# Kernel tuning notes

Measured on AMD Instinct MI355X. Metric: run time of the kernel, lower is better.

The kernel has to match this reference:

```python
import math
import jax, jax.numpy as jnp
import numpy as np

N_EMBD = 1024
N_HEAD = 16
HEAD_DIM = N_EMBD // N_HEAD
B, T = 4, 2048
LN_EPS = 1e-5


def setup_inputs() -> dict:
    key = jax.random.key(0)
    ks = jax.random.split(key, 20)
    s = 0.02
    d = {
        'x': jax.random.normal(ks[0], (B, T, N_EMBD), jnp.float32),
        'Wq': jax.random.normal(ks[1], (N_EMBD, N_EMBD), jnp.float32) * s,
        'bq': jnp.zeros((N_EMBD,), jnp.float32),
        'Wk': jax.random.normal(ks[2], (N_EMBD, N_EMBD), jnp.float32) * s,
        'bk': jnp.zeros((N_EMBD,), jnp.float32),
        'Wv': jax.random.normal(ks[3], (N_EMBD, N_EMBD), jnp.float32) * s,
        'bv': jnp.zeros((N_EMBD,), jnp.float32),
        'Wo': jax.random.normal(ks[4], (N_EMBD, N_EMBD), jnp.float32) * s,
        'bo': jnp.zeros((N_EMBD,), jnp.float32),
        'ln1_g': jnp.ones((N_EMBD,), jnp.float32),
        'ln1_b': jnp.zeros((N_EMBD,), jnp.float32),
        'ln2_g': jnp.ones((N_EMBD,), jnp.float32),
        'ln2_b': jnp.zeros((N_EMBD,), jnp.float32),
        'W_fc': jax.random.normal(ks[5], (N_EMBD, 4 * N_EMBD), jnp.float32) * s,
        'b_fc': jnp.zeros((4 * N_EMBD,), jnp.float32),
        'W_proj': jax.random.normal(ks[6], (4 * N_EMBD, N_EMBD), jnp.float32) * s,
        'b_proj': jnp.zeros((N_EMBD,), jnp.float32),
    }
    return d


def _layernorm(x, g, b):
    mu = jnp.mean(x, axis=-1, keepdims=True)
    var = jnp.var(x, axis=-1, keepdims=True)
    return (x - mu) * jax.lax.rsqrt(var + LN_EPS) * g + b


def _new_gelu(x):
    c = math.sqrt(2.0 / math.pi)
    return 0.5 * x * (1.0 + jnp.tanh(c * (x + 0.044715 * x ** 3)))


def _attn(x, Wq, bq, Wk, bk, Wv, bv, Wo, bo):
    Bq, Tq, C = x.shape
    def heads(y):  # (B,T,C) -> (B,H,T,D)
        return y.reshape(Bq, Tq, N_HEAD, HEAD_DIM).transpose(0, 2, 1, 3)
    q = heads(x @ Wq + bq)
    k = heads(x @ Wk + bk)
    v = heads(x @ Wv + bv)
    scores = jnp.einsum('bhqd,bhkd->bhqk', q, k) / math.sqrt(HEAD_DIM)
    causal = jnp.tril(jnp.ones((Tq, Tq), bool))
    scores = jnp.where(causal, scores, -jnp.inf)
    w = jax.nn.softmax(scores, axis=-1)
    av = jnp.einsum('bhqk,bhkd->bhqd', w, v)
    av = av.transpose(0, 2, 1, 3).reshape(Bq, Tq, C)
    return av @ Wo + bo


def reference(x, Wq, bq, Wk, bk, Wv, bv, Wo, bo, ln1_g, ln1_b, ln2_g, ln2_b, W_fc, b_fc, W_proj, b_proj):
    x = x + _attn(_layernorm(x, ln1_g, ln1_b), Wq, bq, Wk, bk, Wv, bv, Wo, bo)
    h = _layernorm(x, ln2_g, ln2_b)
    x = x + (_new_gelu(h @ W_fc + b_fc) @ W_proj + b_proj)
    return x
```

## Files before the change

kernel.cpp:

```cpp
#include <hip/hip_runtime.h>

typedef __attribute__((ext_vector_type(8))) short short8;
typedef __attribute__((ext_vector_type(4))) short short4v;
typedef __attribute__((ext_vector_type(4))) float floatx4;
typedef unsigned short u16;

#define MFMA16(a,b,c) __builtin_amdgcn_mfma_f32_16x16x32_bf16(a,b,c,0,0,0)

typedef const __attribute__((address_space(1))) void* gas1;
typedef __attribute__((address_space(3))) void* las3;
static __device__ __forceinline__ void glds16(const void* g, void* l){
  __builtin_amdgcn_global_load_lds((gas1)g, (las3)l, 16, 0, 0);
}

static __device__ __forceinline__ u16 f2b(float f){
  union { float f; unsigned int u; } c; c.f = f;
  unsigned int u = c.u;
  u += 0x7fffu + ((u >> 16) & 1u);
  return (u16)(u >> 16);
}

__global__ __launch_bounds__(256) void transpose_cvt(
    const float* __restrict__ W, u16* __restrict__ Wt, int K, int N){
  __shared__ float tile[32][33];
  const int tx = threadIdx.x & 31;
  const int ty = threadIdx.x >> 5;
  const int nx = blockIdx.x * 32, kx = blockIdx.y * 32;
  #pragma unroll
  for (int i = ty; i < 32; i += 8)
    tile[i][tx] = W[(size_t)(kx + i) * N + nx + tx];
  __syncthreads();
  #pragma unroll
  for (int i = ty; i < 32; i += 8)
    Wt[(size_t)(nx + i) * K + kx + tx] = f2b(tile[tx][i]);
}

__global__ __launch_bounds__(256) void ln_kernel(
    const float* __restrict__ x, const float* __restrict__ g,
    const float* __restrict__ b, u16* __restrict__ out){
  const int row = blockIdx.x, tid = threadIdx.x;
  const float4 v = reinterpret_cast<const float4*>(x + (size_t)row * 1024)[tid];
  float s  = v.x + v.y + v.z + v.w;
  float s2 = v.x*v.x + v.y*v.y + v.z*v.z + v.w*v.w;
  #pragma unroll
  for (int off = 1; off < 64; off <<= 1){
    s  += __shfl_xor(s,  off);
    s2 += __shfl_xor(s2, off);
  }
  __shared__ float red[8];
  const int wave = tid >> 6, lane = tid & 63;
  if (lane == 0){ red[wave] = s; red[4 + wave] = s2; }
  __syncthreads();
  s  = red[0] + red[1] + red[2] + red[3];
  s2 = red[4] + red[5] + red[6] + red[7];
  const float mu  = s * (1.f/1024.f);
  const float var = s2 * (1.f/1024.f) - mu * mu;
  const float rs  = rsqrtf(var + 1e-5f);
  const float4 gg = reinterpret_cast<const float4*>(g)[tid];
  const float4 bb = reinterpret_cast<const float4*>(b)[tid];
  ushort4 o;
  o.x = f2b((v.x - mu) * rs * gg.x + bb.x);
  o.y = f2b((v.y - mu) * rs * gg.y + bb.y);
  o.z = f2b((v.z - mu) * rs * gg.z + bb.z);
  o.w = f2b((v.w - mu) * rs * gg.w + bb.w);
  reinterpret_cast<ushort4*>(out + (size_t)row * 1024)[tid] = o;
}

__global__ __launch_bounds__(256) void bias_concat(
    const float* __restrict__ bq, const float* __restrict__ bk,
    const float* __restrict__ bv, float* __restrict__ o){
  const int i = blockIdx.x * 256 + threadIdx.x;
  if (i < 1024) o[i] = bq[i];
  else if (i < 2048) o[i] = bk[i - 1024];
  else if (i < 3072) o[i] = bv[i - 2048];
}

template<bool GELU, bool RES, bool OUTBF, bool QKVMODE>
__global__ __launch_bounds__(256) void gemm128(
    const u16* __restrict__ A, const u16* __restrict__ Bt,
    const float* __restrict__ bias,
    const float* __restrict__ res,
    float* __restrict__ outF, u16* __restrict__ outB,
    u16* __restrict__ vtb,
    int M, int N, int K)
{
  __shared__ __attribute__((aligned(16))) u16 sA[2][128 * 32];
  __shared__ __attribute__((aligned(16))) u16 sB[2][128 * 32];
  const int tid  = threadIdx.x;
  const int wave = tid >> 6, lane = tid & 63, quad = lane >> 4, l16 = lane & 15;
  const int m0 = blockIdx.x * 128, n0 = blockIdx.y * 128;
  const int wm = (wave >> 1) * 64, wn = (wave & 1) * 64;

  const int scol = ((lane & 3) ^ ((lane >> 3) & 3)) * 8;
  const size_t aoff  = (size_t)(m0 + wave*32 + (lane >> 2)) * K + scol;
  const size_t aoff2 = aoff + (size_t)16 * K;
  const int brow = n0 + (wave >> 1)*64 + 4*(lane >> 2) + (wave & 1)*2;
  const size_t boff  = (size_t)brow * K + scol;
  const size_t boff2 = boff + (size_t)K;
  u16* alp = sA[0] + wave * 1024;
  u16* blp = sB[0] + wave * 1024;
  const int qx = (quad ^ ((l16 >> 1) & 3)) * 8;

  floatx4 acc[4][4];
  #pragma unroll
  for (int i = 0; i < 4; i++)
    #pragma unroll
    for (int nt = 0; nt < 4; nt++) acc[i][nt] = floatx4{0.f,0.f,0.f,0.f};

  glds16(A  + aoff,  alp);
  glds16(A  + aoff2, alp + 512);
  glds16(Bt + boff,  blp);
  glds16(Bt + boff2, blp + 512);

  int buf = 0;
  for (int k0 = 0; k0 < K; k0 += 32, buf ^= 1){
    __syncthreads();
    if (k0 + 32 < K){
      const int kn = k0 + 32;
      const int bo = (buf ^ 1) * 4096;
      glds16(A  + aoff  + kn, alp + bo);
      glds16(A  + aoff2 + kn, alp + bo + 512);
      glds16(Bt + boff  + kn, blp + bo);
      glds16(Bt + boff2 + kn, blp + bo + 512);
    }
    const u16* sa = sA[buf];
    const u16* sb = sB[buf];
    short8 af[4], bf[4];
    #pragma unroll
    for (int i = 0; i < 4; i++)
      af[i] = *reinterpret_cast<const short8*>(&sa[(wm + i*16 + l16)*32 + qx]);
    #pragma unroll
    for (int nt = 0; nt < 4; nt++)
      bf[nt] = *reinterpret_cast<const short8*>(&sb[(wn + nt*16 + l16)*32 + qx]);
    #pragma unroll
    for (int i = 0; i < 4; i++)
      #pragma unroll
      for (int nt = 0; nt < 4; nt++)
        acc[i][nt] = MFMA16(af[i], bf[nt], acc[i][nt]);
  }

  const int col0 = n0 + wn + 4*l16;
  const floatx4 bi = *reinterpret_cast<const floatx4*>(&bias[col0]);

  if (QKVMODE && n0 >= 2048){
    #pragma unroll
    for (int nt = 0; nt < 4; nt++){
      const int hd = col0 + nt - 2048;
      u16* vcol = vtb + (size_t)(hd >> 6) * 131072 + (size_t)(hd & 63) * 2048;
      #pragma unroll
      for (int i = 0; i < 4; i++){
        const int t0 = m0 + wm + i*16 + quad*4;
        const int bb = t0 >> 11, tt = t0 & 2047;
        short4v pk;
        #pragma unroll
        for (int r = 0; r < 4; r++) pk[r] = (short)f2b(acc[i][nt][r] + bi[nt]);
        *reinterpret_cast<short4v*>(vcol + (size_t)bb * 2097152 + tt) = pk;
      }
    }
    return;
  }

  #pragma unroll
  for (int i = 0; i < 4; i++){
    #pragma unroll
    for (int r = 0; r < 4; r++){
      const int row = m0 + wm + i*16 + quad*4 + r;
      if (OUTBF){
        short4v o;
        #pragma unroll
        for (int nt = 0; nt < 4; nt++){
          float val = acc[i][nt][r] + bi[nt];
          if (GELU){
            const float t = 0.7978845608028654f * (val + 0.044715f * val * val * val);
            val = val / (1.f + __expf(-2.f * t));
          }
          o[nt] = (short)f2b(val);
        }
        *reinterpret_cast<short4v*>(&outB[(size_t)row * N + col0]) = o;
      } else {
        floatx4 v;
        #pragma unroll
        for (int nt = 0; nt < 4; nt++) v[nt] = acc[i][nt][r] + bi[nt];
        if (RES){
          const floatx4 rr = *reinterpret_cast<const floatx4*>(&res[(size_t)row * N + col0]);
          #pragma unroll
          for (int nt = 0; nt < 4; nt++) v[nt] += rr[nt];
        }
        *reinterpret_cast<floatx4*>(&outF[(size_t)row * N + col0]) = v;
      }
    }
  }
}

__global__ __launch_bounds__(256) void attn_kernel(
    const u16* __restrict__ qkv, const u16* __restrict__ vtb,
    u16* __restrict__ O)
{
  constexpr int T = 2048, LDQ = 3072, LDP = 72;
  __shared__ __attribute__((aligned(16))) u16 sK[2][2][64*32];
  __shared__ __attribute__((aligned(16))) u16 sV[2][2][64*32];
  __shared__ __attribute__((aligned(16))) u16 sP[4][16*LDP];

  const int tid = threadIdx.x, wave = tid >> 6, lane = tid & 63;
  const int quad = lane >> 4, l16 = lane & 15;

  const int lin = blockIdx.y * 16 + blockIdx.x;
  const int j = lin & 15;
  const int bh = lin >> 4;
  const int kk4 = bh >> 4;
  const int jj = (j + ((kk4 & 2) << 2)) & 15;
  const int qt = (kk4 & 1) ? (15 - jj) : jj;
  const int q0 = qt * 128;
  const int b = bh >> 4, h = bh & 15;

  const u16* Qp = qkv + (size_t)b * T * LDQ + h * 64;
  const u16* Kp = Qp + 1024;
  const u16* Vt = vtb + (size_t)bh * 64 * T;

  const int qx = (quad ^ ((l16 >> 1) & 3)) * 8;

  int qg[2]; qg[0] = q0 + wave*16 + l16; qg[1] = qg[0] + 64;
  short8 qf[2][2];
  #pragma unroll
  for (int g = 0; g < 2; g++){
    qf[g][0] = *reinterpret_cast<const short8*>(&Qp[(size_t)qg[g]*LDQ + quad*8]);
    qf[g][1] = *reinterpret_cast<const short8*>(&Qp[(size_t)qg[g]*LDQ + 32 + quad*8]);
  }

  float m_i[2] = {-INFINITY, -INFINITY}, l_i[2] = {0.f, 0.f};
  floatx4 o_acc[2][4];
  #pragma unroll
  for (int g = 0; g < 2; g++)
    #pragma unroll
    for (int nt = 0; nt < 4; nt++) o_acc[g][nt] = floatx4{0.f,0.f,0.f,0.f};

  const int srow = wave*16 + (lane >> 2);
  const int scol = ((lane & 3) ^ ((lane >> 3) & 3)) * 8;
  const int asrc = (lane & 48) | (quad * 4);

  const int kend = q0 + 128;

  {
    glds16(Kp + (size_t)srow*LDQ + scol,      sK[0][0] + wave*512);
    glds16(Kp + (size_t)srow*LDQ + 32 + scol, sK[0][1] + wave*512);
    glds16(Vt + (size_t)srow*T + scol,        sV[0][0] + wave*512);
    glds16(Vt + (size_t)srow*T + 32 + scol,   sV[0][1] + wave*512);
  }

  int buf = 0;
  for (int k0 = 0; k0 < kend; k0 += 64, buf ^= 1){
    __syncthreads();
    if (k0 + 64 < kend){
      const int kn = k0 + 64;
      glds16(Kp + (size_t)(kn + srow)*LDQ + scol,      sK[buf^1][0] + wave*512);
      glds16(Kp + (size_t)(kn + srow)*LDQ + 32 + scol, sK[buf^1][1] + wave*512);
      glds16(Vt + (size_t)srow*T + kn + scol,          sV[buf^1][0] + wave*512);
      glds16(Vt + (size_t)srow*T + kn + 32 + scol,     sV[buf^1][1] + wave*512);
    }

    #pragma unroll
    for (int g = 0; g < 2; g++){
      if (g == 0 && k0 > q0) continue;

      float s[4][4];
      #pragma unroll
      for (int sub = 0; sub < 4; sub++){
        floatx4 sa = floatx4{0.f,0.f,0.f,0.f};
        const short8 kf0 = *reinterpret_cast<const short8*>(&sK[buf][0][(sub*16 + l16)*32 + qx]);
        const short8 kf1 = *reinterpret_cast<const short8*>(&sK[buf][1][(sub*16 + l16)*32 + qx]);
        sa = MFMA16(kf0, qf[g][0], sa);
        sa = MFMA16(kf1, qf[g][1], sa);
        #pragma unroll
        for (int r = 0; r < 4; r++) s[sub][r] = sa[r];
      }
      if (k0 == q0 + g*64){
        #pragma unroll
        for (int sub = 0; sub < 4; sub++)
          #pragma unroll
          for (int r = 0; r < 4; r++){
            const int kidx = k0 + sub*16 + quad*4 + r;
            if (kidx > qg[g]) s[sub][r] = -1e30f;
          }
      }

      float mx = s[0][0];
      #pragma unroll
      for (int sub = 0; sub < 4; sub++)
        #pragma unroll
        for (int r = 0; r < 4; r++) mx = fmaxf(mx, s[sub][r]);
      mx = fmaxf(mx, __shfl_xor(mx, 16));
      mx = fmaxf(mx, __shfl_xor(mx, 32));
      const float mnew  = fmaxf(m_i[g], mx);
      const float alpha = __expf(0.125f * (m_i[g] - mnew));
      float p[4][4], rowsum = 0.f;
      #pragma unroll
      for (int sub = 0; sub < 4; sub++)
        #pragma unroll
        for (int r = 0; r < 4; r++){
          p[sub][r] = __expf(0.125f * (s[sub][r] - mnew));
          rowsum += p[sub][r];
        }
      rowsum += __shfl_xor(rowsum, 16);
      rowsum += __shfl_xor(rowsum, 32);
      l_i[g] = l_i[g] * alpha + rowsum;
      m_i[g] = mnew;

      float arow[4];
      #pragma unroll
      for (int r = 0; r < 4; r++) arow[r] = __shfl(alpha, asrc + r);
      #pragma unroll
      for (int nt = 0; nt < 4; nt++)
        #pragma unroll
        for (int r = 0; r < 4; r++) o_acc[g][nt][r] *= arow[r];

      #pragma unroll
      for (int sub = 0; sub < 4; sub++){
        short4v pk;
        pk[0] = (short)f2b(p[sub][0]); pk[1] = (short)f2b(p[sub][1]);
        pk[2] = (short)f2b(p[sub][2]); pk[3] = (short)f2b(p[sub][3]);
        *reinterpret_cast<short4v*>(&sP[wave][l16*LDP + sub*16 + quad*4]) = pk;
      }
      const short8 pf0 = *reinterpret_cast<const short8*>(&sP[wave][l16*LDP + quad*8]);
      const short8 pf1 = *reinterpret_cast<const short8*>(&sP[wave][l16*LDP + 32 + quad*8]);
      #pragma unroll
      for (int nt = 0; nt < 4; nt++){
        const short8 vf0 = *reinterpret_cast<const short8*>(&sV[buf][0][(nt*16 + l16)*32 + qx]);
        const short8 vf1 = *reinterpret_cast<const short8*>(&sV[buf][1][(nt*16 + l16)*32 + qx]);
        o_acc[g][nt] = MFMA16(pf0, vf0, o_acc[g][nt]);
        o_acc[g][nt] = MFMA16(pf1, vf1, o_acc[g][nt]);
      }
    }
  }

  #pragma unroll
  for (int g = 0; g < 2; g++){
    float lrow[4];
    #pragma unroll
    for (int r = 0; r < 4; r++) lrow[r] = __shfl(l_i[g], asrc + r);
    #pragma unroll
    for (int nt = 0; nt < 4; nt++){
      #pragma unroll
      for (int r = 0; r < 4; r++){
        const int row = q0 + g*64 + wave*16 + quad*4 + r;
        O[(size_t)(b*T + row)*1024 + h*64 + nt*16 + l16] = f2b(o_acc[g][nt][r] / lrow[r]);
      }
    }
  }
}

extern "C" void kernel_launch(void* const* d_in, const int* in_sizes, int n_in,
                              void* d_out, int out_size, void* d_ws, size_t ws_size,
                              hipStream_t stream){
  const float* x      = (const float*)d_in[0];
  const float* Wq     = (const float*)d_in[1];
  const float* bq     = (const float*)d_in[2];
  const float* Wk     = (const float*)d_in[3];
  const float* bk     = (const float*)d_in[4];
  const float* Wv     = (const float*)d_in[5];
  const float* bv     = (const float*)d_in[6];
  const float* Wo     = (const float*)d_in[7];
  const float* bo     = (const float*)d_in[8];
  const float* ln1_g  = (const float*)d_in[9];
  const float* ln1_b  = (const float*)d_in[10];
  const float* ln2_g  = (const float*)d_in[11];
  const float* ln2_b  = (const float*)d_in[12];
  const float* W_fc   = (const float*)d_in[13];
  const float* b_fc   = (const float*)d_in[14];
  const float* W_proj = (const float*)d_in[15];
  const float* b_proj = (const float*)d_in[16];
  float* out = (float*)d_out;
  char* ws = (char*)d_ws;
  const size_t MB = 1024 * 1024;

  u16* bufA  = (u16*)(ws);
  u16* qkvb  = (u16*)(ws + 16*MB);
  u16* vtb   = (u16*)(ws + 64*MB);
  u16* fcb   = (u16*)(ws + 16*MB);
  float* x2  = out;
  u16* Wqkvt = (u16*)(ws + 80*MB);
  u16* Wot   = (u16*)(ws + 86*MB);
  u16* Wfct  = (u16*)(ws + 88*MB);
  u16* Wpjt  = (u16*)(ws + 96*MB);
  float* bqkv= (float*)(ws + 104*MB);

  dim3 tb(256);
  transpose_cvt<<<dim3(32, 32),  tb, 0, stream>>>(Wq,     Wqkvt,             1024, 1024);
  transpose_cvt<<<dim3(32, 32),  tb, 0, stream>>>(Wk,     Wqkvt + 1024*1024, 1024, 1024);
  transpose_cvt<<<dim3(32, 32),  tb, 0, stream>>>(Wv,     Wqkvt + 2048*1024, 1024, 1024);
  transpose_cvt<<<dim3(32, 32),  tb, 0, stream>>>(Wo,     Wot,               1024, 1024);
  transpose_cvt<<<dim3(128, 32), tb, 0, stream>>>(W_fc,   Wfct,              1024, 4096);
  transpose_cvt<<<dim3(32, 128), tb, 0, stream>>>(W_proj, Wpjt,              4096, 1024);
  bias_concat<<<dim3(12), tb, 0, stream>>>(bq, bk, bv, bqkv);

  ln_kernel<<<8192, tb, 0, stream>>>(x, ln1_g, ln1_b, bufA);

  gemm128<false,false,true,true><<<dim3(64,24), tb, 0, stream>>>(
      bufA, Wqkvt, bqkv, nullptr, nullptr, qkvb, vtb, 8192, 3072, 1024);

  attn_kernel<<<dim3(16, 64), tb, 0, stream>>>(qkvb, vtb, bufA);

  gemm128<false,true,false,false><<<dim3(64,8), tb, 0, stream>>>(
      bufA, Wot, bo, x, x2, nullptr, nullptr, 8192, 1024, 1024);

  ln_kernel<<<8192, tb, 0, stream>>>(x2, ln2_g, ln2_b, bufA);

  gemm128<true,false,true,false><<<dim3(64,32), tb, 0, stream>>>(
      bufA, Wfct, b_fc, nullptr, nullptr, fcb, nullptr, 8192, 4096, 1024);

  gemm128<false,true,false,false><<<dim3(64,8), tb, 0, stream>>>(
      fcb, Wpjt, b_proj, x2, out, nullptr, nullptr, 8192, 1024, 4096);
}
```

Measured before the change: 547.2 us.

## Replace 128x128 GEMM with 256x256 tiled 8-wave kernel using fine-grained barrier scheduling

The GEMM kernel moves from a 128x128 tile with 4 waves to a 256x256 tile with 8 waves. Each stage loads a K=64 slice into double-buffered LDS, and the compute is split into interleaved LDS-read and MFMA phases separated by barriers and s_setprio. This raises arithmetic intensity per LDS byte and aims to overlap loads with MFMA. The cost is far fewer blocks (128 for the N=1024 GEMMs), which can leave CUs idle, plus higher register pressure from the 8x4 accumulators.

```diff
diff --git a/kernel.cpp b/kernel.cpp
--- a/kernel.cpp
+++ b/kernel.cpp
@@ -76,7 +76,7 @@
 }
 
 template<bool GELU, bool RES, bool OUTBF, bool QKVMODE>
-__global__ __launch_bounds__(256) void gemm128(
+__global__ __launch_bounds__(512) void gemm256(
     const u16* __restrict__ A, const u16* __restrict__ Bt,
     const float* __restrict__ bias,
     const float* __restrict__ res,
@@ -84,62 +84,93 @@
     u16* __restrict__ vtb,
     int M, int N, int K)
 {
-  __shared__ __attribute__((aligned(16))) u16 sA[2][128 * 32];
-  __shared__ __attribute__((aligned(16))) u16 sB[2][128 * 32];
+  __shared__ __attribute__((aligned(16))) u16 sA[2][2][256 * 32];
+  __shared__ __attribute__((aligned(16))) u16 sB[2][2][256 * 32];
   const int tid  = threadIdx.x;
-  const int wave = tid >> 6, lane = tid & 63, quad = lane >> 4, l16 = lane & 15;
-  const int m0 = blockIdx.x * 128, n0 = blockIdx.y * 128;
-  const int wm = (wave >> 1) * 64, wn = (wave & 1) * 64;
+  const int wave = tid >> 6, lane = tid & 63, ql = lane >> 4, l16 = lane & 15;
+  const int wr = wave >> 2, wc = wave & 3;
+  const int m0 = blockIdx.x * 256, n0 = blockIdx.y * 256;
 
   const int scol = ((lane & 3) ^ ((lane >> 3) & 3)) * 8;
-  const size_t aoff  = (size_t)(m0 + wave*32 + (lane >> 2)) * K + scol;
-  const size_t aoff2 = aoff + (size_t)16 * K;
-  const int brow = n0 + (wave >> 1)*64 + 4*(lane >> 2) + (wave & 1)*2;
-  const size_t boff  = (size_t)brow * K + scol;
-  const size_t boff2 = boff + (size_t)K;
-  u16* alp = sA[0] + wave * 1024;
-  u16* blp = sB[0] + wave * 1024;
-  const int qx = (quad ^ ((l16 >> 1) & 3)) * 8;
-
-  floatx4 acc[4][4];
-  #pragma unroll
-  for (int i = 0; i < 4; i++)
+  const u16* aBase = A  + (size_t)(m0 + wave*16 + (lane >> 2)) * K + scol;
+  const u16* bBase = Bt + (size_t)(n0 + wr*64 + 4*(lane >> 2) + wc) * K + scol;
+  const size_t hK = (size_t)128 * K;
+  const int qx = (ql ^ ((l16 >> 1) & 3)) * 8;
+
+  floatx4 acc[8][4];
+  #pragma unroll
+  for (int i = 0; i < 8; i++)
     #pragma unroll
     for (int nt = 0; nt < 4; nt++) acc[i][nt] = floatx4{0.f,0.f,0.f,0.f};
-
-  glds16(A  + aoff,  alp);
-  glds16(A  + aoff2, alp + 512);
-  glds16(Bt + boff,  blp);
-  glds16(Bt + boff2, blp + 512);
-
-  int buf = 0;
-  for (int k0 = 0; k0 < K; k0 += 32, buf ^= 1){
-    __syncthreads();
-    if (k0 + 32 < K){
-      const int kn = k0 + 32;
-      const int bo = (buf ^ 1) * 4096;
-      glds16(A  + aoff  + kn, alp + bo);
-      glds16(A  + aoff2 + kn, alp + bo + 512);
-      glds16(Bt + boff  + kn, blp + bo);
-      glds16(Bt + boff2 + kn, blp + bo + 512);
-    }
-    const u16* sa = sA[buf];
-    const u16* sb = sB[buf];
-    short8 af[4], bf[4];
-    #pragma unroll
-    for (int i = 0; i < 4; i++)
-      af[i] = *reinterpret_cast<const short8*>(&sa[(wm + i*16 + l16)*32 + qx]);
-    #pragma unroll
-    for (int nt = 0; nt < 4; nt++)
-      bf[nt] = *reinterpret_cast<const short8*>(&sb[(wn + nt*16 + l16)*32 + qx]);
-    #pragma unroll
-    for (int i = 0; i < 4; i++)
-      #pragma unroll
-      for (int nt = 0; nt < 4; nt++)
-        acc[i][nt] = MFMA16(af[i], bf[nt], acc[i][nt]);
-  }
-
-  const int col0 = n0 + wn + 4*l16;
+  short8 af[4], bf[4];
+
+#define STAGE(B_, T_) do { \
+    const size_t ko_ = (size_t)(T_) * 64; \
+    glds16(aBase + ko_,           &sA[B_][0][wave*512]); \
+    glds16(aBase + ko_ + 32,      &sA[B_][1][wave*512]); \
+    glds16(aBase + ko_ + hK,      &sA[B_][0][4096 + wave*512]); \
+    glds16(aBase + ko_ + hK + 32, &sA[B_][1][4096 + wave*512]); \
+    glds16(bBase + ko_,           &sB[B_][0][wave*512]); \
+    glds16(bBase + ko_ + 32,      &sB[B_][1][wave*512]); \
+    glds16(bBase + ko_ + hK,      &sB[B_][0][4096 + wave*512]); \
+    glds16(bBase + ko_ + hK + 32, &sB[B_][1][4096 + wave*512]); \
+  } while(0)
+#define LDA(B_, KH_, Q_) do { \
+    _Pragma("unroll") \
+    for (int ii_ = 0; ii_ < 4; ii_++) \
+      af[ii_] = *reinterpret_cast<const short8*>( \
+          &sA[B_][KH_][(wr*128 + (Q_)*64 + ii_*16 + l16)*32 + qx]); \
+  } while(0)
+#define LDB(B_, KH_) do { \
+    _Pragma("unroll") \
+    for (int nt_ = 0; nt_ < 4; nt_++) \
+      bf[nt_] = *reinterpret_cast<const short8*>( \
+          &sB[B_][KH_][(wc*64 + nt_*16 + l16)*32 + qx]); \
+  } while(0)
+#define MM(Q_) do { \
+    __builtin_amdgcn_s_setprio(1); \
+    _Pragma("unroll") \
+    for (int ii_ = 0; ii_ < 4; ii_++) \
+      _Pragma("unroll") \
+      for (int nt_ = 0; nt_ < 4; nt_++) \
+        acc[(Q_)*4 + ii_][nt_] = MFMA16(af[ii_], bf[nt_], acc[(Q_)*4 + ii_][nt_]); \
+    __builtin_amdgcn_s_setprio(0); \
+  } while(0)
+#define BAR() do { asm volatile("" ::: "memory"); \
+    __builtin_amdgcn_s_barrier(); asm volatile("" ::: "memory"); } while(0)
+#define WAITV(N_) asm volatile("s_waitcnt vmcnt(" #N_ ")" ::: "memory")
+
+  const int ntile = K >> 6;
+  STAGE(0, 0);
+
+  #pragma unroll 1
+  for (int t = 0; t < ntile; t += 2){
+    STAGE(1, t + 1);
+    WAITV(8);
+    BAR();
+    LDB(0, 0); LDA(0, 0, 0); MM(0);
+    BAR();
+    LDA(0, 0, 1); BAR(); MM(1); BAR();
+    LDB(0, 1); LDA(0, 1, 0); BAR(); MM(0); BAR();
+    LDA(0, 1, 1); BAR(); MM(1); BAR();
+    if (t + 2 < ntile){ STAGE(0, t + 2); WAITV(8); }
+    else              { WAITV(0); }
+    BAR();
+    LDB(1, 0); LDA(1, 0, 0); MM(0);
+    BAR();
+    LDA(1, 0, 1); BAR(); MM(1); BAR();
+    LDB(1, 1); LDA(1, 1, 0); BAR(); MM(0); BAR();
+    LDA(1, 1, 1); BAR(); MM(1); BAR();
+  }
+
+#undef STAGE
+#undef LDA
+#undef LDB
+#undef MM
+#undef BAR
+#undef WAITV
+
+  const int col0 = n0 + wc*64 + 4*l16;
   const floatx4 bi = *reinterpret_cast<const floatx4*>(&bias[col0]);
 
   if (QKVMODE && n0 >= 2048){
@@ -148,8 +179,8 @@
       const int hd = col0 + nt - 2048;
       u16* vcol = vtb + (size_t)(hd >> 6) * 131072 + (size_t)(hd & 63) * 2048;
       #pragma unroll
-      for (int i = 0; i < 4; i++){
-        const int t0 = m0 + wm + i*16 + quad*4;
+      for (int i = 0; i < 8; i++){
+        const int t0 = m0 + wr*128 + i*16 + ql*4;
         const int bb = t0 >> 11, tt = t0 & 2047;
         short4v pk;
         #pragma unroll
@@ -161,10 +192,10 @@
   }
 
   #pragma unroll
-  for (int i = 0; i < 4; i++){
+  for (int i = 0; i < 8; i++){
     #pragma unroll
     for (int r = 0; r < 4; r++){
-      const int row = m0 + wm + i*16 + quad*4 + r;
+      const int row = m0 + wr*128 + i*16 + ql*4 + r;
       if (OUTBF){
         short4v o;
         #pragma unroll
@@ -383,7 +414,7 @@
   u16* Wpjt  = (u16*)(ws + 96*MB);
   float* bqkv= (float*)(ws + 104*MB);
 
-  dim3 tb(256);
+  dim3 tb(256), tg(512);
   transpose_cvt<<<dim3(32, 32),  tb, 0, stream>>>(Wq,     Wqkvt,             1024, 1024);
   transpose_cvt<<<dim3(32, 32),  tb, 0, stream>>>(Wk,     Wqkvt + 1024*1024, 1024, 1024);
   transpose_cvt<<<dim3(32, 32),  tb, 0, stream>>>(Wv,     Wqkvt + 2048*1024, 1024, 1024);
@@ -394,19 +425,19 @@
 
   ln_kernel<<<8192, tb, 0, stream>>>(x, ln1_g, ln1_b, bufA);
 
-  gemm128<false,false,true,true><<<dim3(64,24), tb, 0, stream>>>(
+  gemm256<false,false,true,true><<<dim3(32,12), tg, 0, stream>>>(
       bufA, Wqkvt, bqkv, nullptr, nullptr, qkvb, vtb, 8192, 3072, 1024);
 
   attn_kernel<<<dim3(16, 64), tb, 0, stream>>>(qkvb, vtb, bufA);
 
-  gemm128<false,true,false,false><<<dim3(64,8), tb, 0, stream>>>(
+  gemm256<false,true,false,false><<<dim3(32,4), tg, 0, stream>>>(
       bufA, Wot, bo, x, x2, nullptr, nullptr, 8192, 1024, 1024);
 
   ln_kernel<<<8192, tb, 0, stream>>>(x2, ln2_g, ln2_b, bufA);
 
-  gemm128<true,false,true,false><<<dim3(64,32), tb, 0, stream>>>(
+  gemm256<true,false,true,false><<<dim3(32,16), tg, 0, stream>>>(
       bufA, Wfct, b_fc, nullptr, nullptr, fcb, nullptr, 8192, 4096, 1024);
 
-  gemm128<false,true,false,false><<<dim3(64,8), tb, 0, stream>>>(
+  gemm256<false,true,false,false><<<dim3(32,4), tg, 0, stream>>>(
       fcb, Wpjt, b_proj, x2, out, nullptr, nullptr, 8192, 1024, 4096);
 }
```

Result: slower. 616.3 us (+12.6%).
